# Kernel tuning notes

Hardware: AMD Instinct MI355X
Metric: run time of the kernel (lower is better)

Reference implementation:

```python
import jax, jax.numpy as jnp
import numpy as np

N_EMBEDDING = 512
EMBEDDING_DIM = 64
COMMITMENT_COST = 0.25


def setup_inputs() -> dict:
    key = jax.random.key(0)
    k1, k2 = jax.random.split(key)
    inputs = jax.random.normal(k1, (64, 32, 32, EMBEDDING_DIM), dtype=jnp.float32)
    context = jnp.zeros((1,), dtype=jnp.float32)  # unused by the module
    # variance_scaling(1.0, 'fan_in', 'uniform') on shape (D, K): fan_in = D
    limit = np.sqrt(3.0 / EMBEDDING_DIM)
    embeddings = jax.random.uniform(
        k2, (EMBEDDING_DIM, N_EMBEDDING), dtype=jnp.float32,
        minval=-limit, maxval=limit)
    return {"inputs": inputs, "context": context, "embeddings": embeddings}


def reference(inputs, context, embeddings):
    D, K = embeddings.shape
    flat = inputs.reshape(-1, D)  # [N, D]
    distances = (
        jnp.sum(jnp.square(flat), axis=1, keepdims=True)
        - 2.0 * jnp.matmul(flat, embeddings)
        + jnp.sum(jnp.square(embeddings), axis=0, keepdims=True)
    )
    encoding_indices_flat = jnp.argmax(-distances, axis=1)  # [N]
    encodings = jax.nn.one_hot(encoding_indices_flat, K, dtype=distances.dtype)
    encoding_indices = encoding_indices_flat.reshape(inputs.shape[:-1])
    # gather codebook rows: embeddings.T is [K, D]
    quantized = embeddings.T[encoding_indices]  # [B, H, W, D]

    e_latent_loss = jnp.mean(jnp.square(jax.lax.stop_gradient(quantized) - inputs))
    q_latent_loss = jnp.mean(jnp.square(quantized - jax.lax.stop_gradient(inputs)))
    loss = q_latent_loss + COMMITMENT_COST * e_latent_loss

    # straight-through estimator
    quantized = inputs + jax.lax.stop_gradient(quantized - inputs)

    avg_probs = jnp.mean(encodings, axis=0)
    perplexity = jnp.exp(-jnp.sum(avg_probs * jnp.log(avg_probs + 1e-10)))
    return (quantized, loss, perplexity, encodings, encoding_indices, distances)
```

## Files before the change

### kernel.cpp

```cpp
#include <hip/hip_runtime.h>


#define NROWS 65536
#define DIM 64
#define KCODES 512
#define ROWS_PER_BLOCK 128
#define NBLOCKS (NROWS / ROWS_PER_BLOCK)
#define RPT 8

#define QUANT_OFF 0ull
#define LOSS_OFF  4194304ull
#define PERP_OFF  4194305ull
#define ENC_OFF   4194306ull
#define IDX_OFF   37748738ull
#define DIST_OFF  37814274ull

typedef float f32x4 __attribute__((ext_vector_type(4)));

__global__ __launch_bounds__(64) void vq_transpose(
    const float* __restrict__ emb, float* __restrict__ et)
{
    const int t = blockIdx.x * 64 + threadIdx.x;
    f32x4* et4 = (f32x4*)et;
#pragma unroll
    for (int dq = 0; dq < 16; ++dq) {
        f32x4 v;
        v.x = emb[(dq * 4 + 0) * KCODES + t];
        v.y = emb[(dq * 4 + 1) * KCODES + t];
        v.z = emb[(dq * 4 + 2) * KCODES + t];
        v.w = emb[(dq * 4 + 3) * KCODES + t];
        et4[t * 16 + dq] = v;
    }
}

__global__ __launch_bounds__(512, 4) void vq_main(
    const float* __restrict__ inp, const float* __restrict__ emb,
    const float* __restrict__ et,
    float* __restrict__ out, int* __restrict__ hist,
    float* __restrict__ loss_part)
{
    __shared__ f32x4 s_X[ROWS_PER_BLOCK * 16];
    __shared__ float s_sumx2[ROWS_PER_BLOCK];
    __shared__ float s_loss[8];

    const int tid  = threadIdx.x;
    const int w    = tid >> 6;
    const int lane = tid & 63;
    const int rbase = blockIdx.x * ROWS_PER_BLOCK;

    {
        const f32x4* inp4 = (const f32x4*)inp;
#pragma unroll
        for (int i = 0; i < 4; ++i)
            s_X[i * 512 + tid] = inp4[(size_t)blockIdx.x * 2048 + i * 512 + tid];
    }
    __syncthreads();

    {
        const int row_l = w * 16 + (lane >> 2);
        const int q = lane & 3;
        float p = 0.f;
#pragma unroll
        for (int j = 0; j < 4; ++j) {
            const f32x4 v = s_X[row_l * 16 + q * 4 + j];
            p = fmaf(v.x, v.x, p); p = fmaf(v.y, v.y, p);
            p = fmaf(v.z, v.z, p); p = fmaf(v.w, v.w, p);
        }
        p += __shfl_xor(p, 1);
        p += __shfl_xor(p, 2);
        if (q == 0) s_sumx2[row_l] = p;
    }

    f32x4 sume2_0 = {0.f, 0.f, 0.f, 0.f};
    f32x4 sume2_1 = {0.f, 0.f, 0.f, 0.f};
    float loss_acc = 0.f;

    const float* ebase = emb + lane * 4;
    const f32x4* et4 = (const f32x4*)et;

#pragma unroll 1
    for (int g = 0; g < 2; ++g) {
        const int rl0 = w * 16 + g * RPT;

        f32x4 acc[RPT][2];
#pragma unroll
        for (int r = 0; r < RPT; ++r) {
            acc[r][0] = (f32x4){0.f, 0.f, 0.f, 0.f};
            acc[r][1] = (f32x4){0.f, 0.f, 0.f, 0.f};
        }

#pragma unroll 1
        for (int dq = 0; dq < 16; ++dq) {
            f32x4 e0[4], e1[4];
#pragma unroll
            for (int sub = 0; sub < 4; ++sub) {
                e0[sub] = *(const f32x4*)(ebase + (dq * 4 + sub) * KCODES);
                e1[sub] = *(const f32x4*)(ebase + (dq * 4 + sub) * KCODES + 256);
            }
            if (g == 0) {
#pragma unroll
                for (int sub = 0; sub < 4; ++sub) {
                    sume2_0 = sume2_0 + e0[sub] * e0[sub];
                    sume2_1 = sume2_1 + e1[sub] * e1[sub];
                }
            }
#pragma unroll
            for (int r = 0; r < RPT; ++r) {
                const f32x4 xv = s_X[(rl0 + r) * 16 + dq];
                acc[r][0] = acc[r][0] + xv.x * e0[0];
                acc[r][1] = acc[r][1] + xv.x * e1[0];
                acc[r][0] = acc[r][0] + xv.y * e0[1];
                acc[r][1] = acc[r][1] + xv.y * e1[1];
                acc[r][0] = acc[r][0] + xv.z * e0[2];
                acc[r][1] = acc[r][1] + xv.z * e1[2];
                acc[r][0] = acc[r][0] + xv.w * e0[3];
                acc[r][1] = acc[r][1] + xv.w * e1[3];
            }
        }

#pragma unroll
        for (int r = 0; r < RPT; ++r) {
            const int row = rbase + rl0 + r;
            const float sx2 = s_sumx2[rl0 + r];

            const f32x4 dd0 = (sume2_0 + sx2) + (-2.f) * acc[r][0];
            const f32x4 dd1 = (sume2_1 + sx2) + (-2.f) * acc[r][1];

            f32x4* dp = (f32x4*)(out + DIST_OFF) + (size_t)row * 128;
            __builtin_nontemporal_store(dd0, dp + lane);
            __builtin_nontemporal_store(dd1, dp + 64 + lane);

            float bd = fminf(fminf(fminf(dd0.x, dd0.y), fminf(dd0.z, dd0.w)),
                             fminf(fminf(dd1.x, dd1.y), fminf(dd1.z, dd1.w)));
            const int kb = lane * 4;
            int ck = 0x7fffffff;
            if (dd1.w == bd) ck = 256 + kb + 3;
            if (dd1.z == bd) ck = 256 + kb + 2;
            if (dd1.y == bd) ck = 256 + kb + 1;
            if (dd1.x == bd) ck = 256 + kb + 0;
            if (dd0.w == bd) ck = kb + 3;
            if (dd0.z == bd) ck = kb + 2;
            if (dd0.y == bd) ck = kb + 1;
            if (dd0.x == bd) ck = kb + 0;

            float fd = bd;
#pragma unroll
            for (int off = 32; off; off >>= 1)
                fd = fminf(fd, __shfl_xor(fd, off));
            int c2 = (bd == fd) ? ck : 0x7fffffff;
#pragma unroll
            for (int off = 32; off; off >>= 1) {
                const int ok = __shfl_xor(c2, off);
                c2 = ok < c2 ? ok : c2;
            }

            f32x4* ep = (f32x4*)(out + ENC_OFF) + (size_t)row * 128;
            const int cq = c2 >> 2;
            f32x4 v0 = {0.f, 0.f, 0.f, 0.f};
            f32x4 v1 = {0.f, 0.f, 0.f, 0.f};
            if (cq == lane) {
                v0.x = (c2 & 3) == 0 ? 1.f : 0.f;
                v0.y = (c2 & 3) == 1 ? 1.f : 0.f;
                v0.z = (c2 & 3) == 2 ? 1.f : 0.f;
                v0.w = (c2 & 3) == 3 ? 1.f : 0.f;
            }
            if (cq == 64 + lane) {
                v1.x = (c2 & 3) == 0 ? 1.f : 0.f;
                v1.y = (c2 & 3) == 1 ? 1.f : 0.f;
                v1.z = (c2 & 3) == 2 ? 1.f : 0.f;
                v1.w = (c2 & 3) == 3 ? 1.f : 0.f;
            }
            __builtin_nontemporal_store(v0, ep + lane);
            __builtin_nontemporal_store(v1, ep + 64 + lane);

            if (lane < 16) {
                const f32x4 q = et4[c2 * 16 + lane];
                ((f32x4*)(out + QUANT_OFF + (size_t)row * DIM))[lane] = q;
            }

            if (lane == 0) {
                out[IDX_OFF + row] = (float)c2;
                atomicAdd(&hist[c2], 1);
                loss_acc += fd;
            }
        }
    }

    if (lane == 0) s_loss[w] = loss_acc;
    __syncthreads();
    if (tid == 0) {
        float s = 0.f;
#pragma unroll
        for (int i = 0; i < 8; ++i) s += s_loss[i];
        loss_part[blockIdx.x] = s;
    }
}

__global__ __launch_bounds__(512) void vq_final(
    const int* __restrict__ hist, const float* __restrict__ loss_part,
    float* __restrict__ out)
{
    __shared__ float s_red[8];
    __shared__ float s_red2[8];
    const int tid = threadIdx.x;
    const int w = tid >> 6, lane = tid & 63;

    float p = (float)hist[tid] * (1.f / 65536.f);
    float t = p * logf(p + 1e-10f);
    float l = loss_part[tid];
#pragma unroll
    for (int off = 32; off; off >>= 1) {
        t += __shfl_xor(t, off);
        l += __shfl_xor(l, off);
    }
    if (lane == 0) { s_red[w] = t; s_red2[w] = l; }
    __syncthreads();
    if (tid == 0) {
        float s = 0.f, ls = 0.f;
#pragma unroll
        for (int i = 0; i < 8; ++i) { s += s_red[i]; ls += s_red2[i]; }
        out[PERP_OFF] = expf(-s);
        out[LOSS_OFF] = ls * (1.25f / 4194304.f);
    }
}

extern "C" void kernel_launch(void* const* d_in, const int* in_sizes, int n_in,
                              void* d_out, int out_size, void* d_ws, size_t ws_size,
                              hipStream_t stream) {
    const float* inp = (const float*)d_in[0];
    const float* emb = (const float*)d_in[2];
    float* out = (float*)d_out;
    int*   hist      = (int*)d_ws;
    float* loss_part = (float*)((char*)d_ws + 2048);
    float* et        = (float*)((char*)d_ws + 8192);

    (void)hipMemsetAsync(d_ws, 0, 2048, stream);
    vq_transpose<<<dim3(8), dim3(64), 0, stream>>>(emb, et);
    vq_main<<<dim3(NBLOCKS), dim3(512), 0, stream>>>(
        inp, emb, et, out, hist, loss_part);
    vq_final<<<dim3(1), dim3(512), 0, stream>>>(hist, loss_part, out);
}
```

Measured before the change: 104.6 us.

## Move histogram to final kernel, shrink row groups, stagger groups, use regular stores

```diff
diff --git a/kernel.cpp b/kernel.cpp
--- a/kernel.cpp
+++ b/kernel.cpp
@@ -6,7 +6,8 @@
 #define KCODES 512
 #define ROWS_PER_BLOCK 128
 #define NBLOCKS (NROWS / ROWS_PER_BLOCK)
-#define RPT 8
+#define RPT 4
+#define NGRP 4
 
 #define QUANT_OFF 0ull
 #define LOSS_OFF  4194304ull
@@ -36,8 +37,7 @@
 __global__ __launch_bounds__(512, 4) void vq_main(
     const float* __restrict__ inp, const float* __restrict__ emb,
     const float* __restrict__ et,
-    float* __restrict__ out, int* __restrict__ hist,
-    float* __restrict__ loss_part)
+    float* __restrict__ out, float* __restrict__ loss_part)
 {
     __shared__ f32x4 s_X[ROWS_PER_BLOCK * 16];
     __shared__ float s_sumx2[ROWS_PER_BLOCK];
@@ -79,7 +79,8 @@
     const f32x4* et4 = (const f32x4*)et;
 
 #pragma unroll 1
-    for (int g = 0; g < 2; ++g) {
+    for (int gi = 0; gi < NGRP; ++gi) {
+        const int g   = (gi + w) & 3;
         const int rl0 = w * 16 + g * RPT;
 
         f32x4 acc[RPT][2];
@@ -97,7 +98,7 @@
                 e0[sub] = *(const f32x4*)(ebase + (dq * 4 + sub) * KCODES);
                 e1[sub] = *(const f32x4*)(ebase + (dq * 4 + sub) * KCODES + 256);
             }
-            if (g == 0) {
+            if (gi == 0) {
 #pragma unroll
                 for (int sub = 0; sub < 4; ++sub) {
                     sume2_0 = sume2_0 + e0[sub] * e0[sub];
@@ -127,8 +128,8 @@
             const f32x4 dd1 = (sume2_1 + sx2) + (-2.f) * acc[r][1];
 
             f32x4* dp = (f32x4*)(out + DIST_OFF) + (size_t)row * 128;
-            __builtin_nontemporal_store(dd0, dp + lane);
-            __builtin_nontemporal_store(dd1, dp + 64 + lane);
+            dp[lane]      = dd0;
+            dp[64 + lane] = dd1;
 
             float bd = fminf(fminf(fminf(dd0.x, dd0.y), fminf(dd0.z, dd0.w)),
                              fminf(fminf(dd1.x, dd1.y), fminf(dd1.z, dd1.w)));
@@ -170,8 +171,8 @@
                 v1.z = (c2 & 3) == 2 ? 1.f : 0.f;
                 v1.w = (c2 & 3) == 3 ? 1.f : 0.f;
             }
-            __builtin_nontemporal_store(v0, ep + lane);
-            __builtin_nontemporal_store(v1, ep + 64 + lane);
+            ep[lane]      = v0;
+            ep[64 + lane] = v1;
 
             if (lane < 16) {
                 const f32x4 q = et4[c2 * 16 + lane];
@@ -180,7 +181,6 @@
 
             if (lane == 0) {
                 out[IDX_OFF + row] = (float)c2;
-                atomicAdd(&hist[c2], 1);
                 loss_acc += fd;
             }
         }
@@ -197,15 +197,32 @@
 }
 
 __global__ __launch_bounds__(512) void vq_final(
-    const int* __restrict__ hist, const float* __restrict__ loss_part,
+    const float* __restrict__ out_ro, const float* __restrict__ loss_part,
     float* __restrict__ out)
 {
+    __shared__ int   s_hist[8][KCODES];
     __shared__ float s_red[8];
     __shared__ float s_red2[8];
     const int tid = threadIdx.x;
     const int w = tid >> 6, lane = tid & 63;
 
-    float p = (float)hist[tid] * (1.f / 65536.f);
+#pragma unroll
+    for (int i = 0; i < 8; ++i) ((int*)s_hist)[i * 512 + tid] = 0;
+    __syncthreads();
+
+    const float* idx_f = out_ro + IDX_OFF;
+#pragma unroll 4
+    for (int i = 0; i < 128; ++i) {
+        const int idx = (int)idx_f[i * 512 + tid];
+        atomicAdd(&s_hist[w][idx], 1);
+    }
+    __syncthreads();
+
+    int cnt = 0;
+#pragma unroll
+    for (int h = 0; h < 8; ++h) cnt += s_hist[h][tid];
+
+    float p = (float)cnt * (1.f / 65536.f);
     float t = p * logf(p + 1e-10f);
     float l = loss_part[tid];
 #pragma unroll
@@ -230,13 +247,11 @@
     const float* inp = (const float*)d_in[0];
     const float* emb = (const float*)d_in[2];
     float* out = (float*)d_out;
-    int*   hist      = (int*)d_ws;
     float* loss_part = (float*)((char*)d_ws + 2048);
     float* et        = (float*)((char*)d_ws + 8192);
 
-    (void)hipMemsetAsync(d_ws, 0, 2048, stream);
     vq_transpose<<<dim3(8), dim3(64), 0, stream>>>(emb, et);
     vq_main<<<dim3(NBLOCKS), dim3(512), 0, stream>>>(
-        inp, emb, et, out, hist, loss_part);
-    vq_final<<<dim3(1), dim3(512), 0, stream>>>(hist, loss_part, out);
-}
+        inp, emb, et, out, loss_part);
+    vq_final<<<dim3(1), dim3(512), 0, stream>>>(out, loss_part, out);
+}
```

Result: slower. 140.7 us (+34.6%).
